# Kernel tuning notes

Hardware: AMD Instinct MI355X
Metric: run time of the kernel (lower is better)

## Reference

```python
import jax, jax.numpy as jnp
import numpy as np

NUM_ENT = 10000
NUM_REL = 230
S_DIM = 96
T_DIM = 32
DIM = S_DIM + T_DIM  # 128
N = 32768   # neighbors
Q = 4096    # unique query entities
E = 32768   # pooling edges
B = 1024    # batch triples
BN_EPS = 1e-5


def setup_inputs() -> dict:
    key = jax.random.key(0)
    ks = jax.random.split(key, 32)
    inp = {}
    inp["neighbor_idx"] = jax.random.randint(ks[0], (N,), 0, NUM_ENT)
    inp["rel_id"] = jax.random.randint(ks[1], (N,), 0, 2 * NUM_REL)
    inp["years"] = jax.random.uniform(ks[2], (N, 1), jnp.float32)
    inp["months"] = jax.random.uniform(ks[3], (N, 1), jnp.float32)
    inp["days"] = jax.random.uniform(ks[4], (N, 1), jnp.float32)
    inp["pool_src"] = jax.random.randint(ks[5], (E,), 0, N)
    inp["pool_dst"] = jax.random.randint(ks[6], (E,), 0, Q)
    inp["head_pos"] = jax.random.randint(ks[7], (B,), 0, Q)
    inp["tail_pos"] = jax.random.randint(ks[8], (B,), 0, Q)
    inp["rels"] = jax.random.randint(ks[9], (B,), 0, NUM_REL)
    # parameters (xavier-ish scales)
    inp["ent_embs"] = jax.random.normal(ks[10], (NUM_ENT, S_DIM), jnp.float32) * 0.05
    names = ["y_freq", "y_phi", "y_amp", "m_freq", "m_phi", "m_amp", "d_freq", "d_phi", "d_amp"]
    for i, n in enumerate(names):
        inp[n] = jax.random.normal(ks[11 + i], (NUM_ENT, T_DIM), jnp.float32) * 0.05
    inp["rel_embs"] = jax.random.normal(ks[20], (NUM_REL, DIM), jnp.float32) * 0.05
    inp["W"] = jax.random.normal(ks[21], (2 * NUM_REL, DIM, DIM), jnp.float32) * (1.0 / np.sqrt(DIM))
    inp["b"] = jnp.zeros((2 * NUM_REL, DIM), jnp.float32)
    inp["gamma"] = jnp.ones((2 * NUM_REL, DIM), jnp.float32)
    inp["beta"] = jnp.zeros((2 * NUM_REL, DIM), jnp.float32)
    return inp


def _forward(ent_embs, y_freq, y_phi, y_amp, m_freq, m_phi, m_amp,
             d_freq, d_phi, d_amp, rel_embs, W, b, gamma, beta,
             years, months, days,
             neighbor_idx, rel_id, pool_src, pool_dst, head_pos, tail_pos, rels):
    # diachronic time embedding: amp * sin(freq * t + phi), summed over y/m/d
    ty = y_amp[neighbor_idx] * jnp.sin(y_freq[neighbor_idx] * years + y_phi[neighbor_idx])
    tm = m_amp[neighbor_idx] * jnp.sin(m_freq[neighbor_idx] * months + m_phi[neighbor_idx])
    td = d_amp[neighbor_idx] * jnp.sin(d_freq[neighbor_idx] * days + d_phi[neighbor_idx])
    x = jnp.concatenate([ent_embs[neighbor_idx], ty + tm + td], axis=1)  # [N, DIM]

    # per-relation Linear (gather weights per neighbor)
    z = jnp.einsum('nd,nde->ne', x, W[rel_id]) + b[rel_id]  # [N, DIM]

    # per-relation-bucket BatchNorm (training stats, biased var); skipped for singleton buckets
    R2 = 2 * NUM_REL
    cnt = jax.ops.segment_sum(jnp.ones((z.shape[0],), z.dtype), rel_id, num_segments=R2)
    denom = jnp.maximum(cnt, 1.0)[:, None]
    mean = jax.ops.segment_sum(z, rel_id, num_segments=R2) / denom
    var = jax.ops.segment_sum(z * z, rel_id, num_segments=R2) / denom - mean * mean
    var = jnp.maximum(var, 0.0)
    zn = (z - mean[rel_id]) * jax.lax.rsqrt(var[rel_id] + BN_EPS) * gamma[rel_id] + beta[rel_id]
    z = jnp.where((cnt[rel_id] > 1.0)[:, None], zn, z)
    z = jax.nn.relu(z)

    # average pooling of neighbor features per query entity (PoolingLayer 'avg')
    psum = jax.ops.segment_sum(z[pool_src], pool_dst, num_segments=Q)
    pcnt = jax.ops.segment_sum(jnp.ones((pool_src.shape[0],), z.dtype), pool_dst, num_segments=Q)
    emb = psum / jnp.maximum(pcnt, 1.0)[:, None]  # [Q, DIM]

    # TransE-style scoring: -||h + r - t||_2 (dropout p=0 / eval mode)
    diff = emb[head_pos] + rel_embs[rels] - emb[tail_pos]
    return -jnp.sqrt(jnp.sum(diff * diff, axis=1))


def reference(neighbor_idx, rel_id, years, months, days, pool_src, pool_dst,
              head_pos, tail_pos, rels, ent_embs, y_freq, y_phi, y_amp,
              m_freq, m_phi, m_amp, d_freq, d_phi, d_amp, rel_embs, W, b, gamma, beta):
    return _forward(ent_embs, y_freq, y_phi, y_amp, m_freq, m_phi, m_amp,
                    d_freq, d_phi, d_amp, rel_embs, W, b, gamma, beta,
                    years, months, days,
                    neighbor_idx, rel_id, pool_src, pool_dst, head_pos, tail_pos, rels)
```

## Files before the change

kernel.cpp:

```cpp
#include <hip/hip_runtime.h>
#include <math.h>

#define NUM_ENT 10000
#define NUM_REL 230
#define R2      460
#define S_DIM   96
#define T_DIM   32
#define DIM     128
#define N_NBR   32768
#define Q_ENT   4096
#define E_EDGE  32768
#define B_TRI   1024
#define BN_EPS  1e-5f
#define CHUNK   64
#define ZCAP    128
#define WQB     (R2 * 4)

typedef __attribute__((ext_vector_type(8))) short bf16x8;
typedef __attribute__((ext_vector_type(4))) float f32x4;

__device__ __forceinline__ unsigned short f2bf(float f) {
    unsigned int u = __float_as_uint(f);
    u = (u + 0x7FFFu + ((u >> 16) & 1u)) >> 16;
    return (unsigned short)u;
}
__device__ __forceinline__ float bf2f(unsigned short us) {
    return __uint_as_float((unsigned int)us << 16);
}

__device__ __forceinline__ int XIDX(int m, int d) {
    return (m * DIM + d) ^ ((m & 7) << 3);
}

__global__ void k_zero(int* __restrict__ p, int n4) {
    int i = blockIdx.x * blockDim.x + threadIdx.x;
    if (i < n4) ((int4*)p)[i] = make_int4(0, 0, 0, 0);
}

__global__ __launch_bounds__(256) void k_front(
    const float* __restrict__ W, unsigned short* __restrict__ Wfrag,
    const int* __restrict__ rel, const int* __restrict__ pdst,
    int* __restrict__ hist_rel, int* __restrict__ hist_dst,
    int* __restrict__ ticket_n, int* __restrict__ ticket_d)
{
    const int t = threadIdx.x;
    if (blockIdx.x >= WQB) {
        const int i = (blockIdx.x - WQB) * 256 + t;
        if (i < N_NBR) ticket_n[i] = atomicAdd(&hist_rel[rel[i]], 1);
        if (i < E_EDGE) ticket_d[i] = atomicAdd(&hist_dst[pdst[i]], 1);
        return;
    }
    const int r = blockIdx.x >> 2;
    const int p = blockIdx.x & 3;
    __shared__ __align__(16) float Xf[32 * DIM];
    {
        const float4* Wg = (const float4*)(W + (size_t)r * DIM * DIM + p * 32 * DIM);
        float4* Xf4 = (float4*)Xf;
        #pragma unroll
        for (int i = 0; i < 4; ++i)
            Xf4[t + i * 256] = Wg[t + i * 256];
    }
    __syncthreads();
    unsigned short* dst = Wfrag + (size_t)r * DIM * DIM;
    #pragma unroll
    for (int i = 0; i < 2; ++i) {
        const int id  = p * 512 + t + i * 256;
        const int lane = id & 63;
        const int h    = (id >> 6) & 1;
        const int wv   = (id >> 7) & 3;
        const int n  = 32 * wv + 16 * h + (lane & 15);
        const int kb = 8 * (lane >> 4);
        ushort4 lo, hi;
        lo.x = f2bf(Xf[(kb + 0) * DIM + n]);
        lo.y = f2bf(Xf[(kb + 1) * DIM + n]);
        lo.z = f2bf(Xf[(kb + 2) * DIM + n]);
        lo.w = f2bf(Xf[(kb + 3) * DIM + n]);
        hi.x = f2bf(Xf[(kb + 4) * DIM + n]);
        hi.y = f2bf(Xf[(kb + 5) * DIM + n]);
        hi.z = f2bf(Xf[(kb + 6) * DIM + n]);
        hi.w = f2bf(Xf[(kb + 7) * DIM + n]);
        *(ushort4*)&dst[id * 8]     = lo;
        *(ushort4*)&dst[id * 8 + 4] = hi;
    }
}

__global__ __launch_bounds__(256) void k_place(
    const int* __restrict__ rel, const int* __restrict__ psrc,
    const int* __restrict__ pdst,
    const int* __restrict__ hist_rel, const int* __restrict__ hist_dst,
    const int* __restrict__ ticket_n, const int* __restrict__ ticket_d,
    int* __restrict__ offsets, int* __restrict__ dst_off,
    int* __restrict__ order, int* __restrict__ drow)
{
    __shared__ int hA[512], hD[4096], part[256];
    const int t = threadIdx.x;
    const int b = blockIdx.x;

    hA[t]       = (t < R2) ? hist_rel[t] : 0;
    hA[t + 256] = (t + 256 < R2) ? hist_rel[t + 256] : 0;
    #pragma unroll
    for (int j = 0; j < 16; ++j) hD[t + j * 256] = hist_dst[t + j * 256];
    __syncthreads();

    const int a0 = hA[2 * t], a1 = hA[2 * t + 1];
    part[t] = a0 + a1;
    __syncthreads();
    for (int off = 1; off < 256; off <<= 1) {
        int v = (t >= off) ? part[t - off] : 0;
        __syncthreads();
        part[t] += v;
        __syncthreads();
    }
    {
        const int ex = t ? part[t - 1] : 0;
        hA[2 * t] = ex; hA[2 * t + 1] = ex + a0;
        if (b == 0) {
            if (2 * t < R2)     offsets[2 * t]     = ex;
            if (2 * t + 1 < R2) offsets[2 * t + 1] = ex + a0;
            if (t == 255)       offsets[R2]        = part[255];
        }
    }
    __syncthreads();

    {
        const int base = t * 16;
        int v[16]; int lsum = 0;
        #pragma unroll
        for (int j = 0; j < 16; ++j) { v[j] = hD[base + j]; lsum += v[j]; }
        part[t] = lsum;
        __syncthreads();
        for (int off = 1; off < 256; off <<= 1) {
            int vv = (t >= off) ? part[t - off] : 0;
            __syncthreads();
            part[t] += vv;
            __syncthreads();
        }
        int run = t ? part[t - 1] : 0;
        #pragma unroll
        for (int j = 0; j < 16; ++j) {
            hD[base + j] = run;
            if (b == 0) dst_off[base + j] = run;
            run += v[j];
        }
        if (b == 0 && t == 255) dst_off[4096] = run;
    }
    __syncthreads();

    const int i = b * 256 + t;
    if (i < N_NBR) {
        order[hA[rel[i]] + ticket_n[i]] = i;
    }
    if (i < E_EDGE) {
        const int s = psrc[i];
        const int row  = hA[rel[s]] + ticket_n[s];
        const int dpos = hD[pdst[i]] + ticket_d[i];
        drow[dpos] = row;
    }
}

__global__ __launch_bounds__(512, 4) void k_matvec(
    const int* __restrict__ order, const int* __restrict__ offsets,
    const int* __restrict__ nbr,
    const float* __restrict__ years, const float* __restrict__ months, const float* __restrict__ days,
    const float* __restrict__ ent,
    const float* __restrict__ yf, const float* __restrict__ yp, const float* __restrict__ ya,
    const float* __restrict__ mf, const float* __restrict__ mp, const float* __restrict__ ma,
    const float* __restrict__ df, const float* __restrict__ dp, const float* __restrict__ da,
    const unsigned short* __restrict__ Wfrag, const float* __restrict__ bias,
    const float* __restrict__ gamma, const float* __restrict__ beta,
    unsigned short* __restrict__ zf)
{
    const int r     = blockIdx.x;
    const int start = offsets[r];
    const int cnt   = offsets[r + 1] - start;
    if (cnt == 0) return;

    __shared__ __align__(16) unsigned short Xl[2][CHUNK * DIM];
    __shared__ __align__(16) unsigned short Zl[ZCAP * DIM];
    __shared__ int s_ord[2][CHUNK];
    __shared__ int s_ni[2][CHUNK];
    __shared__ float bnred[8][2][16][2];
    __shared__ float scl[DIM], shf[DIM];

    const int t    = threadIdx.x;
    const int wid  = t >> 6;
    const int half = wid >> 2;
    const int wv   = wid & 3;
    const int lane = t & 63;
    const int l15  = lane & 15;
    const int g    = lane >> 4;

    const int nn0 = 32 * wv + l15;
    const int nn1 = nn0 + 16;
    const float bv0 = bias[r * DIM + nn0];
    const float bv1 = bias[r * DIM + nn1];

    float lsum0 = 0.f, lsq0 = 0.f, lsum1 = 0.f, lsq1 = 0.f;
    const unsigned short* Wr = Wfrag + (size_t)r * DIM * DIM;

    for (int cbase = 0; cbase < cnt; cbase += 2 * CHUNK) {
        const int hbase = cbase + half * CHUNK;
        const int mcnt  = min(CHUNK, max(0, cnt - hbase));

        if (t < 2 * CHUNK) {
            const int hh = t >> 6;
            const int m  = t & 63;
            const int gb = cbase + hh * CHUNK;
            int o = -1, ni = 0;
            if (gb + m < cnt) { o = order[start + gb + m]; ni = nbr[o]; }
            s_ord[hh][m] = o;
            s_ni[hh][m]  = ni;
        }
        __syncthreads();

        if (mcnt > 0) {
            const int lt = t & 255;
            const int m = lt >> 2, s = lt & 3;
            const int ni = s_ni[half][m];
            const bool vm = (m < mcnt);
            #pragma unroll
            for (int kk = 0; kk < 6; ++kk) {
                const int d = 4 * (s + 4 * kk);
                float4 e = *(const float4*)(ent + (size_t)ni * S_DIM + d);
                ushort4 b;
                b.x = vm ? f2bf(e.x) : 0; b.y = vm ? f2bf(e.y) : 0;
                b.z = vm ? f2bf(e.z) : 0; b.w = vm ? f2bf(e.w) : 0;
                *(ushort4*)&Xl[half][XIDX(m, d)] = b;
            }
            const int o = s_ord[half][m] < 0 ? 0 : s_ord[half][m];
            const float yr = years[o], mo = months[o], dy = days[o];
            #pragma unroll
            for (int hh = 0; hh < 2; ++hh) {
                const int j0 = s * 8 + hh * 4;
                const size_t tb = (size_t)ni * T_DIM + j0;
                const float4 vyf = *(const float4*)(yf + tb), vyp = *(const float4*)(yp + tb), vya = *(const float4*)(ya + tb);
                const float4 vmf = *(const float4*)(mf + tb), vmp = *(const float4*)(mp + tb), vma = *(const float4*)(ma + tb);
                const float4 vdf = *(const float4*)(df + tb), vdp = *(const float4*)(dp + tb), vda = *(const float4*)(da + tb);
                ushort4 b;
                #pragma unroll
                for (int j = 0; j < 4; ++j) {
                    const float fy = ((const float*)&vyf)[j] * yr + ((const float*)&vyp)[j];
                    const float fm = ((const float*)&vmf)[j] * mo + ((const float*)&vmp)[j];
                    const float fd = ((const float*)&vdf)[j] * dy + ((const float*)&vdp)[j];
                    float v = ((const float*)&vya)[j] * sinf(fy)
                            + ((const float*)&vma)[j] * sinf(fm)
                            + ((const float*)&vda)[j] * sinf(fd);
                    ((unsigned short*)&b)[j] = vm ? f2bf(v) : 0;
                }
                *(ushort4*)&Xl[half][XIDX(m, S_DIM + j0)] = b;
            }
        }
        __syncthreads();

        if (mcnt > 0) {
            f32x4 acc[4][2];
            #pragma unroll
            for (int i = 0; i < 4; ++i)
                #pragma unroll
                for (int j = 0; j < 2; ++j) acc[i][j] = (f32x4)0.f;

            #pragma unroll
            for (int kk = 0; kk < 4; ++kk) {
                const int k0 = kk * 32;
                bf16x8 a[4];
                #pragma unroll
                for (int mt = 0; mt < 4; ++mt)
                    a[mt] = *(const bf16x8*)&Xl[half][XIDX(16 * mt + l15, k0 + 8 * g)];
                const bf16x8 b0 = *(const bf16x8*)&Wr[(size_t)((kk * 4 + wv) * 2 + 0) * 512 + lane * 8];
                const bf16x8 b1 = *(const bf16x8*)&Wr[(size_t)((kk * 4 + wv) * 2 + 1) * 512 + lane * 8];
                #pragma unroll
                for (int mt = 0; mt < 4; ++mt) {
                    acc[mt][0] = __builtin_amdgcn_mfma_f32_16x16x32_bf16(a[mt], b0, acc[mt][0], 0, 0, 0);
                    acc[mt][1] = __builtin_amdgcn_mfma_f32_16x16x32_bf16(a[mt], b1, acc[mt][1], 0, 0, 0);
                }
            }

            #pragma unroll
            for (int mt = 0; mt < 4; ++mt) {
                #pragma unroll
                for (int reg = 0; reg < 4; ++reg) {
                    const int ml = 16 * mt + 4 * g + reg;
                    if (ml < mcnt) {
                        const float v0 = acc[mt][0][reg] + bv0;
                        const float v1 = acc[mt][1][reg] + bv1;
                        const int lrow = hbase + ml;
                        if (lrow < ZCAP) {
                            Zl[lrow * DIM + nn0] = f2bf(v0);
                            Zl[lrow * DIM + nn1] = f2bf(v1);
                        } else {
                            const size_t row = (size_t)(start + lrow) * DIM;
                            zf[row + nn0] = f2bf(v0);
                            zf[row + nn1] = f2bf(v1);
                        }
                        lsum0 += v0; lsq0 += v0 * v0;
                        lsum1 += v1; lsq1 += v1 * v1;
                    }
                }
            }
        }
        __syncthreads();
    }

    lsum0 += __shfl_xor(lsum0, 16); lsum0 += __shfl_xor(lsum0, 32);
    lsq0  += __shfl_xor(lsq0, 16);  lsq0  += __shfl_xor(lsq0, 32);
    lsum1 += __shfl_xor(lsum1, 16); lsum1 += __shfl_xor(lsum1, 32);
    lsq1  += __shfl_xor(lsq1, 16);  lsq1  += __shfl_xor(lsq1, 32);
    if (g == 0) {
        bnred[wid][0][l15][0] = lsum0; bnred[wid][0][l15][1] = lsq0;
        bnred[wid][1][l15][0] = lsum1; bnred[wid][1][l15][1] = lsq1;
    }
    __syncthreads();
    if (half == 0 && g == 0) {
        #pragma unroll
        for (int nt = 0; nt < 2; ++nt) {
            const int col = 32 * wv + 16 * nt + l15;
            const float s = bnred[wid][nt][l15][0] + bnred[wid + 4][nt][l15][0];
            const float q = bnred[wid][nt][l15][1] + bnred[wid + 4][nt][l15][1];
            float sc = 1.f, sh = 0.f;
            if (cnt > 1) {
                const float mean = s / (float)cnt;
                const float var  = fmaxf(q / (float)cnt - mean * mean, 0.f);
                const int gi = r * DIM + col;
                sc = gamma[gi] * rsqrtf(var + BN_EPS);
                sh = beta[gi] - mean * sc;
            }
            scl[col] = sc;
            shf[col] = sh;
        }
    }
    __syncthreads();

    {
        const int d2 = (t & 63) * 2;
        const int grp = t >> 6;
        const float sc0 = scl[d2],     sh0 = shf[d2];
        const float sc1 = scl[d2 + 1], sh1 = shf[d2 + 1];
        const int nrows = min(cnt, ZCAP);
        for (int i = grp; i < nrows; i += 8) {
            const ushort2 zz = *(const ushort2*)&Zl[i * DIM + d2];
            ushort2 o;
            o.x = f2bf(fmaxf(bf2f(zz.x) * sc0 + sh0, 0.f));
            o.y = f2bf(fmaxf(bf2f(zz.y) * sc1 + sh1, 0.f));
            *(ushort2*)&zf[(size_t)(start + i) * DIM + d2] = o;
        }
        for (int i = ZCAP + grp; i < cnt; i += 8) {
            const size_t base = (size_t)(start + i) * DIM + d2;
            const ushort2 zz = *(const ushort2*)&zf[base];
            ushort2 o;
            o.x = f2bf(fmaxf(bf2f(zz.x) * sc0 + sh0, 0.f));
            o.y = f2bf(fmaxf(bf2f(zz.y) * sc1 + sh1, 0.f));
            *(ushort2*)&zf[base] = o;
        }
    }
}

__global__ void k_score(const int* __restrict__ head, const int* __restrict__ tail,
                        const int* __restrict__ rels,
                        const unsigned short* __restrict__ zf,
                        const int* __restrict__ drow, const int* __restrict__ dst_off,
                        const float* __restrict__ rel_embs,
                        float* __restrict__ out)
{
    const int b = blockIdx.x;
    const int t = threadIdx.x;
    const int d2 = t * 2;
    const int h = head[b], tq = tail[b], r = rels[b];

    const int h0 = dst_off[h],  h1 = dst_off[h + 1];
    const int t0 = dst_off[tq], t1 = dst_off[tq + 1];

    float fh0 = 0.f, fh1 = 0.f;
    for (int e = h0; e < h1; ++e) {
        const ushort2 v = *(const ushort2*)&zf[(size_t)drow[e] * DIM + d2];
        fh0 += bf2f(v.x); fh1 += bf2f(v.y);
    }
    const float hn = 1.f / (float)max(h1 - h0, 1);
    fh0 *= hn; fh1 *= hn;

    float ft0 = 0.f, ft1 = 0.f;
    for (int e = t0; e < t1; ++e) {
        const ushort2 v = *(const ushort2*)&zf[(size_t)drow[e] * DIM + d2];
        ft0 += bf2f(v.x); ft1 += bf2f(v.y);
    }
    const float tn = 1.f / (float)max(t1 - t0, 1);
    ft0 *= tn; ft1 *= tn;

    const float2 re = *(const float2*)&rel_embs[r * DIM + d2];
    const float d0 = fh0 + re.x - ft0;
    const float d1 = fh1 + re.y - ft1;
    float sq = d0 * d0 + d1 * d1;
    for (int off = 32; off > 0; off >>= 1) sq += __shfl_down(sq, off);
    if (t == 0) out[b] = -sqrtf(sq);
}

extern "C" void kernel_launch(void* const* d_in, const int* in_sizes, int n_in,
                              void* d_out, int out_size, void* d_ws, size_t ws_size,
                              hipStream_t stream) {
    const int*   neighbor_idx = (const int*)  d_in[0];
    const int*   rel_id       = (const int*)  d_in[1];
    const float* years        = (const float*)d_in[2];
    const float* months       = (const float*)d_in[3];
    const float* days         = (const float*)d_in[4];
    const int*   pool_src     = (const int*)  d_in[5];
    const int*   pool_dst     = (const int*)  d_in[6];
    const int*   head_pos     = (const int*)  d_in[7];
    const int*   tail_pos     = (const int*)  d_in[8];
    const int*   rels         = (const int*)  d_in[9];
    const float* ent_embs     = (const float*)d_in[10];
    const float* y_freq       = (const float*)d_in[11];
    const float* y_phi        = (const float*)d_in[12];
    const float* y_amp        = (const float*)d_in[13];
    const float* m_freq       = (const float*)d_in[14];
    const float* m_phi        = (const float*)d_in[15];
    const float* m_amp        = (const float*)d_in[16];
    const float* d_freq       = (const float*)d_in[17];
    const float* d_phi        = (const float*)d_in[18];
    const float* d_amp        = (const float*)d_in[19];
    const float* rel_embs     = (const float*)d_in[20];
    const float* W            = (const float*)d_in[21];
    const float* bias         = (const float*)d_in[22];
    const float* gamma        = (const float*)d_in[23];
    const float* beta         = (const float*)d_in[24];

    float* out = (float*)d_out;

    float* ws = (float*)d_ws;
    size_t off = 0;
    unsigned short* Wfrag = (unsigned short*)(ws + off); off += (size_t)R2 * DIM * DIM / 2;
    unsigned short* zf    = (unsigned short*)(ws + off); off += (size_t)N_NBR * DIM / 2;
    int* hist_rel = (int*)(ws + off); off += R2;
    int* hist_dst = (int*)(ws + off); off += Q_ENT;
    int* ticket_n = (int*)(ws + off); off += N_NBR;
    int* ticket_d = (int*)(ws + off); off += E_EDGE;
    int* offsets  = (int*)(ws + off); off += R2 + 1;
    int* dst_off  = (int*)(ws + off); off += Q_ENT + 1;
    int* order    = (int*)(ws + off); off += N_NBR;
    int* drow     = (int*)(ws + off); off += E_EDGE;

    const int nzero  = R2 + Q_ENT;
    const int nzero4 = (nzero + 3) / 4;
    k_zero<<<(nzero4 + 255) / 256, 256, 0, stream>>>(hist_rel, nzero4);

    k_front<<<WQB + (N_NBR + 255) / 256, 256, 0, stream>>>(
        W, Wfrag, rel_id, pool_dst,
        hist_rel, hist_dst, ticket_n, ticket_d);

    k_place<<<(N_NBR + 255) / 256, 256, 0, stream>>>(
        rel_id, pool_src, pool_dst, hist_rel, hist_dst,
        ticket_n, ticket_d, offsets, dst_off, order, drow);

    k_matvec<<<R2, 512, 0, stream>>>(order, offsets,
                                     neighbor_idx,
                                     years, months, days, ent_embs,
                                     y_freq, y_phi, y_amp,
                                     m_freq, m_phi, m_amp,
                                     d_freq, d_phi, d_amp,
                                     Wfrag, bias, gamma, beta,
                                     zf);

    k_score<<<B_TRI, 64, 0, stream>>>(head_pos, tail_pos, rels,
                                      zf, drow, dst_off, rel_embs, out);
}
```

Before: 66.85 us.

## Split matvec columns across all eight waves with single-chunk staging

The per-relation matvec kernel now stages one 64-row chunk at a time, and each of the 8 waves computes 16 output columns. Previously two half-blocks each took a 64-row chunk and every wave computed 32 columns. This drops the cross-half BN reduction buffer and one barrier, and halves the MFMA accumulators per wave. In exchange the number of chunk iterations and barriers doubles for relations with many neighbors, and the A fragments are reloaded from LDS by every wave.

```diff
diff --git a/kernel.cpp b/kernel.cpp
--- a/kernel.cpp
+++ b/kernel.cpp
@@ -175,89 +175,74 @@
     const int cnt   = offsets[r + 1] - start;
     if (cnt == 0) return;
 
-    __shared__ __align__(16) unsigned short Xl[2][CHUNK * DIM];
+    __shared__ __align__(16) unsigned short Xl[CHUNK * DIM];
     __shared__ __align__(16) unsigned short Zl[ZCAP * DIM];
-    __shared__ int s_ord[2][CHUNK];
-    __shared__ int s_ni[2][CHUNK];
-    __shared__ float bnred[8][2][16][2];
+    __shared__ int s_ord[CHUNK];
+    __shared__ int s_ni[CHUNK];
     __shared__ float scl[DIM], shf[DIM];
 
     const int t    = threadIdx.x;
     const int wid  = t >> 6;
-    const int half = wid >> 2;
-    const int wv   = wid & 3;
     const int lane = t & 63;
     const int l15  = lane & 15;
     const int g    = lane >> 4;
 
-    const int nn0 = 32 * wv + l15;
-    const int nn1 = nn0 + 16;
-    const float bv0 = bias[r * DIM + nn0];
-    const float bv1 = bias[r * DIM + nn1];
-
-    float lsum0 = 0.f, lsq0 = 0.f, lsum1 = 0.f, lsq1 = 0.f;
+    const int col = 16 * wid + l15;
+    const float bv = bias[r * DIM + col];
+    float lsum = 0.f, lsq = 0.f;
+
     const unsigned short* Wr = Wfrag + (size_t)r * DIM * DIM;
 
-    for (int cbase = 0; cbase < cnt; cbase += 2 * CHUNK) {
-        const int hbase = cbase + half * CHUNK;
-        const int mcnt  = min(CHUNK, max(0, cnt - hbase));
-
-        if (t < 2 * CHUNK) {
-            const int hh = t >> 6;
-            const int m  = t & 63;
-            const int gb = cbase + hh * CHUNK;
+    for (int cbase = 0; cbase < cnt; cbase += CHUNK) {
+        const int mcnt = min(CHUNK, cnt - cbase);
+
+        if (t < CHUNK) {
             int o = -1, ni = 0;
-            if (gb + m < cnt) { o = order[start + gb + m]; ni = nbr[o]; }
-            s_ord[hh][m] = o;
-            s_ni[hh][m]  = ni;
-        }
-        __syncthreads();
-
-        if (mcnt > 0) {
-            const int lt = t & 255;
-            const int m = lt >> 2, s = lt & 3;
-            const int ni = s_ni[half][m];
+            if (cbase + t < cnt) { o = order[start + cbase + t]; ni = nbr[o]; }
+            s_ord[t] = o;
+            s_ni[t]  = ni;
+        }
+        __syncthreads();
+
+        {
+            const int m = t >> 3, s2 = t & 7;
+            const int ni = s_ni[m];
             const bool vm = (m < mcnt);
             #pragma unroll
-            for (int kk = 0; kk < 6; ++kk) {
-                const int d = 4 * (s + 4 * kk);
+            for (int kk = 0; kk < 3; ++kk) {
+                const int d = 4 * (s2 + 8 * kk);
                 float4 e = *(const float4*)(ent + (size_t)ni * S_DIM + d);
                 ushort4 b;
                 b.x = vm ? f2bf(e.x) : 0; b.y = vm ? f2bf(e.y) : 0;
                 b.z = vm ? f2bf(e.z) : 0; b.w = vm ? f2bf(e.w) : 0;
-                *(ushort4*)&Xl[half][XIDX(m, d)] = b;
+                *(ushort4*)&Xl[XIDX(m, d)] = b;
             }
-            const int o = s_ord[half][m] < 0 ? 0 : s_ord[half][m];
+            const int o = s_ord[m] < 0 ? 0 : s_ord[m];
             const float yr = years[o], mo = months[o], dy = days[o];
+            const int j0 = s2 * 4;
+            const size_t tb = (size_t)ni * T_DIM + j0;
+            const float4 vyf = *(const float4*)(yf + tb), vyp = *(const float4*)(yp + tb), vya = *(const float4*)(ya + tb);
+            const float4 vmf = *(const float4*)(mf + tb), vmp = *(const float4*)(mp + tb), vma = *(const float4*)(ma + tb);
+            const float4 vdf = *(const float4*)(df + tb), vdp = *(const float4*)(dp + tb), vda = *(const float4*)(da + tb);
+            ushort4 b;
             #pragma unroll
-            for (int hh = 0; hh < 2; ++hh) {
-                const int j0 = s * 8 + hh * 4;
-                const size_t tb = (size_t)ni * T_DIM + j0;
-                const float4 vyf = *(const float4*)(yf + tb), vyp = *(const float4*)(yp + tb), vya = *(const float4*)(ya + tb);
-                const float4 vmf = *(const float4*)(mf + tb), vmp = *(const float4*)(mp + tb), vma = *(const float4*)(ma + tb);
-                const float4 vdf = *(const float4*)(df + tb), vdp = *(const float4*)(dp + tb), vda = *(const float4*)(da + tb);
-                ushort4 b;
-                #pragma unroll
-                for (int j = 0; j < 4; ++j) {
-                    const float fy = ((const float*)&vyf)[j] * yr + ((const float*)&vyp)[j];
-                    const float fm = ((const float*)&vmf)[j] * mo + ((const float*)&vmp)[j];
-                    const float fd = ((const float*)&vdf)[j] * dy + ((const float*)&vdp)[j];
-                    float v = ((const float*)&vya)[j] * sinf(fy)
-                            + ((const float*)&vma)[j] * sinf(fm)
-                            + ((const float*)&vda)[j] * sinf(fd);
-                    ((unsigned short*)&b)[j] = vm ? f2bf(v) : 0;
-                }
-                *(ushort4*)&Xl[half][XIDX(m, S_DIM + j0)] = b;
+            for (int j = 0; j < 4; ++j) {
+                const float fy = ((const float*)&vyf)[j] * yr + ((const float*)&vyp)[j];
+                const float fm = ((const float*)&vmf)[j] * mo + ((const float*)&vmp)[j];
+                const float fd = ((const float*)&vdf)[j] * dy + ((const float*)&vdp)[j];
+                float v = ((const float*)&vya)[j] * sinf(fy)
+                        + ((const float*)&vma)[j] * sinf(fm)
+                        + ((const float*)&vda)[j] * sinf(fd);
+                ((unsigned short*)&b)[j] = vm ? f2bf(v) : 0;
             }
-        }
-        __syncthreads();
-
-        if (mcnt > 0) {
-            f32x4 acc[4][2];
+            *(ushort4*)&Xl[XIDX(m, S_DIM + j0)] = b;
+        }
+        __syncthreads();
+
+        {
+            f32x4 acc[4];
             #pragma unroll
-            for (int i = 0; i < 4; ++i)
-                #pragma unroll
-                for (int j = 0; j < 2; ++j) acc[i][j] = (f32x4)0.f;
+            for (int i = 0; i < 4; ++i) acc[i] = (f32x4)0.f;
 
             #pragma unroll
             for (int kk = 0; kk < 4; ++kk) {
@@ -265,14 +250,11 @@
                 bf16x8 a[4];
                 #pragma unroll
                 for (int mt = 0; mt < 4; ++mt)
-                    a[mt] = *(const bf16x8*)&Xl[half][XIDX(16 * mt + l15, k0 + 8 * g)];
-                const bf16x8 b0 = *(const bf16x8*)&Wr[(size_t)((kk * 4 + wv) * 2 + 0) * 512 + lane * 8];
-                const bf16x8 b1 = *(const bf16x8*)&Wr[(size_t)((kk * 4 + wv) * 2 + 1) * 512 + lane * 8];
+                    a[mt] = *(const bf16x8*)&Xl[XIDX(16 * mt + l15, k0 + 8 * g)];
+                const bf16x8 bfr = *(const bf16x8*)&Wr[(size_t)((kk * 4 + (wid >> 1)) * 2 + (wid & 1)) * 512 + lane * 8];
                 #pragma unroll
-                for (int mt = 0; mt < 4; ++mt) {
-                    acc[mt][0] = __builtin_amdgcn_mfma_f32_16x16x32_bf16(a[mt], b0, acc[mt][0], 0, 0, 0);
-                    acc[mt][1] = __builtin_amdgcn_mfma_f32_16x16x32_bf16(a[mt], b1, acc[mt][1], 0, 0, 0);
-                }
+                for (int mt = 0; mt < 4; ++mt)
+                    acc[mt] = __builtin_amdgcn_mfma_f32_16x16x32_bf16(a[mt], bfr, acc[mt], 0, 0, 0);
             }
 
             #pragma unroll
@@ -281,19 +263,15 @@
                 for (int reg = 0; reg < 4; ++reg) {
                     const int ml = 16 * mt + 4 * g + reg;
                     if (ml < mcnt) {
-                        const float v0 = acc[mt][0][reg] + bv0;
-                        const float v1 = acc[mt][1][reg] + bv1;
-                        const int lrow = hbase + ml;
+                        const float v = acc[mt][reg] + bv;
+                        const int lrow = cbase + ml;
                         if (lrow < ZCAP) {
-                            Zl[lrow * DIM + nn0] = f2bf(v0);
-                            Zl[lrow * DIM + nn1] = f2bf(v1);
+                            Zl[lrow * DIM + col] = f2bf(v);
                         } else {
-                            const size_t row = (size_t)(start + lrow) * DIM;
-                            zf[row + nn0] = f2bf(v0);
-                            zf[row + nn1] = f2bf(v1);
+                            zf[(size_t)(start + lrow) * DIM + col] = f2bf(v);
                         }
-                        lsum0 += v0; lsq0 += v0 * v0;
-                        lsum1 += v1; lsq1 += v1 * v1;
+                        lsum += v;
+                        lsq  += v * v;
                     }
                 }
             }
@@ -301,32 +279,19 @@
         __syncthreads();
     }
 
-    lsum0 += __shfl_xor(lsum0, 16); lsum0 += __shfl_xor(lsum0, 32);
-    lsq0  += __shfl_xor(lsq0, 16);  lsq0  += __shfl_xor(lsq0, 32);
-    lsum1 += __shfl_xor(lsum1, 16); lsum1 += __shfl_xor(lsum1, 32);
-    lsq1  += __shfl_xor(lsq1, 16);  lsq1  += __shfl_xor(lsq1, 32);
+    lsum += __shfl_xor(lsum, 16); lsum += __shfl_xor(lsum, 32);
+    lsq  += __shfl_xor(lsq, 16);  lsq  += __shfl_xor(lsq, 32);
     if (g == 0) {
-        bnred[wid][0][l15][0] = lsum0; bnred[wid][0][l15][1] = lsq0;
-        bnred[wid][1][l15][0] = lsum1; bnred[wid][1][l15][1] = lsq1;
-    }
-    __syncthreads();
-    if (half == 0 && g == 0) {
-        #pragma unroll
-        for (int nt = 0; nt < 2; ++nt) {
-            const int col = 32 * wv + 16 * nt + l15;
-            const float s = bnred[wid][nt][l15][0] + bnred[wid + 4][nt][l15][0];
-            const float q = bnred[wid][nt][l15][1] + bnred[wid + 4][nt][l15][1];
-            float sc = 1.f, sh = 0.f;
-            if (cnt > 1) {
-                const float mean = s / (float)cnt;
-                const float var  = fmaxf(q / (float)cnt - mean * mean, 0.f);
-                const int gi = r * DIM + col;
-                sc = gamma[gi] * rsqrtf(var + BN_EPS);
-                sh = beta[gi] - mean * sc;
-            }
-            scl[col] = sc;
-            shf[col] = sh;
-        }
+        float sc = 1.f, sh = 0.f;
+        if (cnt > 1) {
+            const float mean = lsum / (float)cnt;
+            const float var  = fmaxf(lsq / (float)cnt - mean * mean, 0.f);
+            const int gi = r * DIM + col;
+            sc = gamma[gi] * rsqrtf(var + BN_EPS);
+            sh = beta[gi] - mean * sc;
+        }
+        scl[col] = sc;
+        shf[col] = sh;
     }
     __syncthreads();
 
```

Measured after the change: 66.36 us. Within noise of the previous version (-0.7%).
